# Kernel optimization log

Measured on AMD Instinct MI355X. Metric: run time of the kernel, lower is better.

Reference implementation:

```python
import jax, jax.numpy as jnp
import numpy as np

B, T, D = 2, 2048, 4096
H = 32            # query heads
HKV = 1           # kv heads (MQA; torch code requires HKV in {1, H})
HD = D // H       # head_dim = 128


def setup_inputs() -> dict:
    key = jax.random.key(0)
    ks = jax.random.split(key, 9)
    s = lambda fan_in: 1.0 / np.sqrt(fan_in)
    return {
        "x": jax.random.normal(ks[0], (B, T, D), dtype=jnp.float32),
        "wq_w": jax.random.normal(ks[1], (H * HD, D), dtype=jnp.float32) * s(D),
        "wq_b": jax.random.normal(ks[2], (H * HD,), dtype=jnp.float32) * 0.02,
        "wk_w": jax.random.normal(ks[3], (HKV * HD, D), dtype=jnp.float32) * s(D),
        "wk_b": jax.random.normal(ks[4], (HKV * HD,), dtype=jnp.float32) * 0.02,
        "wv_w": jax.random.normal(ks[5], (HKV * HD, D), dtype=jnp.float32) * s(D),
        "wv_b": jax.random.normal(ks[6], (HKV * HD,), dtype=jnp.float32) * 0.02,
        "wo_w": jax.random.normal(ks[7], (D, H * HD), dtype=jnp.float32) * s(H * HD),
        "wo_b": jax.random.normal(ks[8], (D,), dtype=jnp.float32) * 0.02,
    }


def reference(x, wq_w, wq_b, wk_w, wk_b, wv_w, wv_b, wo_w, wo_b):
    b, t, d = x.shape
    # projections (torch Linear: y = x @ W.T + b)
    q = (x @ wq_w.T + wq_b).reshape(b, t, H, HD)        # [B,T,H,hd]
    k = (x @ wk_w.T + wk_b).reshape(b, t, HKV, HD)      # [B,T,HKV,hd]
    v = (x @ wv_w.T + wv_b).reshape(b, t, HKV, HD)
    # MQA: squeeze the single kv head and broadcast across query heads
    k1 = k[:, :, 0, :]                                   # [B,T,hd]
    v1 = v[:, :, 0, :]
    scores = jnp.einsum("bqhd,bkd->bhqk", q, k1) / jnp.sqrt(jnp.float32(HD))
    causal = jnp.tril(jnp.ones((t, t), dtype=bool))      # keep lower triangle
    scores = jnp.where(causal, scores, -jnp.inf)
    weights = jax.nn.softmax(scores, axis=-1)            # [B,H,T,T]
    attn = jnp.einsum("bhqk,bkd->bqhd", weights, v1)     # [B,T,H,hd]
    attn = attn.reshape(b, t, H * HD)
    return attn @ wo_w.T + wo_b
```

## Files before the change

kernel.cpp:

```cpp
#include <hip/hip_runtime.h>

typedef unsigned short u16;
using bf16x8 = __attribute__((ext_vector_type(8))) __bf16;
using f32x4  = __attribute__((ext_vector_type(4))) float;


__device__ __forceinline__ u16 f2b(float f) {
    union { float f; unsigned int i; } x; x.f = f;
    unsigned int i = x.i + (((x.i >> 16) & 1u) + 0x7fffu);
    return (u16)(i >> 16);
}
__device__ __forceinline__ u16 f2b_ru(float f) {
    union { float f; unsigned int i; } x; x.f = f;
    return (u16)((x.i + 0x8000u) >> 16);
}
__device__ __forceinline__ void gload_lds16(const u16* g, u16* l) {
    __builtin_amdgcn_global_load_lds((const __attribute__((address_space(1))) void*)g,
                                     (__attribute__((address_space(3))) void*)l, 16, 0, 0);
}

__global__ __launch_bounds__(256) void cvt_f32_bf16(const float* __restrict__ in,
                                                    u16* __restrict__ out, int n) {
    int i = (blockIdx.x * 256 + threadIdx.x) * 8;
    if (i >= n) return;
    float4 a = *(const float4*)(in + i);
    float4 b = *(const float4*)(in + i + 4);
    union { u16 u[8]; uint4 v; } o;
    o.u[0] = f2b(a.x); o.u[1] = f2b(a.y); o.u[2] = f2b(a.z); o.u[3] = f2b(a.w);
    o.u[4] = f2b(b.x); o.u[5] = f2b(b.y); o.u[6] = f2b(b.z); o.u[7] = f2b(b.w);
    *(uint4*)(out + i) = o.v;
}


#define G_BAR()   __builtin_amdgcn_s_barrier()
#define G_LGKM0() asm volatile("s_waitcnt lgkmcnt(0)" ::: "memory")

struct GCtx {
    const u16* gA; const u16* gB;
    int fro;
    int dst;
    int wmi, wni;
    int rgA0, rgA1, rgB0, rgB1;
    int w;
};

__device__ __forceinline__ void stg2(const GCtx& c, const u16* gb, int rg, int kt, u16* sb) {
    const u16* src = gb + (size_t)rg * 65536 + (size_t)kt * 64;
    u16* d = sb + rg * 1024 + c.dst;
    gload_lds16(src,      d);
    gload_lds16(src + 32, d + 512);
}

template<int MODE>
__device__ __forceinline__ void tile_step(const GCtx& c, int u,
        u16* __restrict__ cA, u16* __restrict__ cB,
        u16* __restrict__ nA, u16* __restrict__ nB,
        f32x4 (&acc)[8][4]) {
    bf16x8 af[4][2], bf[2][2];
#pragma unroll
    for (int i = 0; i < 4; ++i) {
        const u16* p = cA + (((c.wmi * 8 + i) * 2) << 9) + c.fro;
        af[i][0] = *(const bf16x8*)(p);
        af[i][1] = *(const bf16x8*)(p + 512);
    }
#pragma unroll
    for (int n = 0; n < 2; ++n) {
        const u16* p = cB + (((c.wni * 4 + n) * 2) << 9) + c.fro;
        bf[n][0] = *(const bf16x8*)(p);
        bf[n][1] = *(const bf16x8*)(p + 512);
    }
    if (MODE < 2) stg2(c, c.gA, c.rgA1, u + 1, nA);
    G_BAR(); G_LGKM0();
    __builtin_amdgcn_s_setprio(1);
#pragma unroll
    for (int i = 0; i < 4; ++i)
#pragma unroll
        for (int n = 0; n < 2; ++n) {
            acc[i][n] = __builtin_amdgcn_mfma_f32_16x16x32_bf16(af[i][0], bf[n][0], acc[i][n], 0, 0, 0);
            acc[i][n] = __builtin_amdgcn_mfma_f32_16x16x32_bf16(af[i][1], bf[n][1], acc[i][n], 0, 0, 0);
        }
    __builtin_amdgcn_s_setprio(0);
    G_BAR();
#pragma unroll
    for (int n = 0; n < 2; ++n) {
        const u16* p = cB + (((c.wni * 4 + 2 + n) * 2) << 9) + c.fro;
        bf[n][0] = *(const bf16x8*)(p);
        bf[n][1] = *(const bf16x8*)(p + 512);
    }
    if (MODE < 2) stg2(c, c.gB, c.rgB0, u + 1, nB);
    G_BAR(); G_LGKM0();
    __builtin_amdgcn_s_setprio(1);
#pragma unroll
    for (int i = 0; i < 4; ++i)
#pragma unroll
        for (int n = 0; n < 2; ++n) {
            acc[i][2 + n] = __builtin_amdgcn_mfma_f32_16x16x32_bf16(af[i][0], bf[n][0], acc[i][2 + n], 0, 0, 0);
            acc[i][2 + n] = __builtin_amdgcn_mfma_f32_16x16x32_bf16(af[i][1], bf[n][1], acc[i][2 + n], 0, 0, 0);
        }
    __builtin_amdgcn_s_setprio(0);
    G_BAR();
#pragma unroll
    for (int i = 0; i < 4; ++i) {
        const u16* p = cA + (((c.wmi * 8 + 4 + i) * 2) << 9) + c.fro;
        af[i][0] = *(const bf16x8*)(p);
        af[i][1] = *(const bf16x8*)(p + 512);
    }
    if (MODE == 0) stg2(c, c.gA, c.rgA0, u + 2, cA);
    G_BAR(); G_LGKM0();
    __builtin_amdgcn_s_setprio(1);
#pragma unroll
    for (int i = 0; i < 4; ++i)
#pragma unroll
        for (int n = 0; n < 2; ++n) {
            acc[4 + i][2 + n] = __builtin_amdgcn_mfma_f32_16x16x32_bf16(af[i][0], bf[n][0], acc[4 + i][2 + n], 0, 0, 0);
            acc[4 + i][2 + n] = __builtin_amdgcn_mfma_f32_16x16x32_bf16(af[i][1], bf[n][1], acc[4 + i][2 + n], 0, 0, 0);
        }
    __builtin_amdgcn_s_setprio(0);
    G_BAR();
#pragma unroll
    for (int n = 0; n < 2; ++n) {
        const u16* p = cB + (((c.wni * 4 + n) * 2) << 9) + c.fro;
        bf[n][0] = *(const bf16x8*)(p);
        bf[n][1] = *(const bf16x8*)(p + 512);
    }
    if (MODE == 0) stg2(c, c.gB, c.rgB1, u + 2, cB);
    G_BAR(); G_LGKM0();
    __builtin_amdgcn_s_setprio(1);
#pragma unroll
    for (int i = 0; i < 4; ++i)
#pragma unroll
        for (int n = 0; n < 2; ++n) {
            acc[4 + i][n] = __builtin_amdgcn_mfma_f32_16x16x32_bf16(af[i][0], bf[n][0], acc[4 + i][n], 0, 0, 0);
            acc[4 + i][n] = __builtin_amdgcn_mfma_f32_16x16x32_bf16(af[i][1], bf[n][1], acc[4 + i][n], 0, 0, 0);
        }
    __builtin_amdgcn_s_setprio(0);
    if (MODE == 0) asm volatile("s_waitcnt vmcnt(4)" ::: "memory");
    if (MODE == 1) asm volatile("s_waitcnt vmcnt(0)" ::: "memory");
    G_BAR();
}

template<int NT>
__device__ __forceinline__ void gemm256(const u16* __restrict__ Ag,
                                        const u16* __restrict__ Bg,
                                        u16* __restrict__ lds,
                                        f32x4 (&acc)[8][4]) {
    const int t = threadIdx.x, l = t & 63, w = t >> 6;
    const int r = l & 15, qd = l >> 4, lr = l >> 2;
    const int co = ((l & 3) * 8) ^ (((l >> 5) & 1) << 4);
    GCtx c;
    c.w = w; c.wmi = w >> 2; c.wni = w & 3;
    c.gA = Ag + (size_t)lr * 4096 + co;
    c.gB = Bg + (size_t)lr * 4096 + co;
    c.fro = r * 32 + ((qd * 8) ^ (((r >> 3) & 1) << 4));
    c.dst = l * 8;
    c.rgA0 = (w & 3) | ((w & 4) << 1);
    c.rgA1 = c.rgA0 + 4;
    c.rgB0 = (w & 1) | ((w >> 1) << 2);
    c.rgB1 = c.rgB0 + 2;
    u16* sA0 = lds;          u16* sB0 = lds + 16384;
    u16* sA1 = lds + 32768;  u16* sB1 = lds + 49152;
#pragma unroll
    for (int i = 0; i < 8; ++i)
#pragma unroll
        for (int n = 0; n < 4; ++n) acc[i][n] = (f32x4){0.f, 0.f, 0.f, 0.f};
    stg2(c, c.gA, w, 0, sA0);     stg2(c, c.gA, w + 8, 0, sA0);
    stg2(c, c.gB, w, 0, sB0);     stg2(c, c.gB, w + 8, 0, sB0);
    stg2(c, c.gA, c.rgA0, 1, sA1);
    stg2(c, c.gB, c.rgB1, 1, sB1);
    asm volatile("s_waitcnt vmcnt(4)" ::: "memory");
    G_BAR();
#pragma unroll 1
    for (int u = 0; u + 2 < NT; u += 2) {
        tile_step<0>(c, u,     sA0, sB0, sA1, sB1, acc);
        tile_step<0>(c, u + 1, sA1, sB1, sA0, sB0, acc);
    }
    tile_step<1>(c, NT - 2, sA0, sB0, sA1, sB1, acc);
    tile_step<2>(c, NT - 1, sA1, sB1, sA0, sB0, acc);
}

__global__ __launch_bounds__(512, 2) void q_gemm(
    const u16* __restrict__ x, const u16* __restrict__ wq,
    const float* __restrict__ wqb, u16* __restrict__ Qb) {
    __shared__ __align__(16) u16 lds[65536];
    int bid = blockIdx.x;
    int wgid = (bid & 7) * 32 + (bid >> 3);
    int brow = wgid >> 4, bcol = wgid & 15;
    f32x4 acc[8][4];
    gemm256<64>(x + (size_t)brow * 256 * 4096, wq + (size_t)bcol * 256 * 4096, lds, acc);
    const int t = threadIdx.x, l = t & 63, w = t >> 6;
    const int wmi = w >> 2, wni = w & 3, r = l & 15, qd = l >> 4;
    const float QSCALE = 0.08838834764831845f * 1.4426950408889634f;
#pragma unroll
    for (int n = 0; n < 4; ++n) {
        int col = bcol * 256 + wni * 64 + n * 16 + r;
        float bv = wqb[col];
#pragma unroll
        for (int mt = 0; mt < 8; ++mt)
#pragma unroll
            for (int j = 0; j < 4; ++j) {
                int m = brow * 256 + wmi * 128 + mt * 16 + qd * 4 + j;
                Qb[(size_t)m * 4096 + col] = f2b((acc[mt][n][j] + bv) * QSCALE);
            }
    }
}

__global__ __launch_bounds__(512, 2) void kv_gemm(
    const u16* __restrict__ x, const u16* __restrict__ wkv,
    float* __restrict__ P) {
    __shared__ __align__(16) u16 lds[65536];
    int brow = blockIdx.x;
    int slice = blockIdx.y;
    f32x4 acc[8][4];
    gemm256<8>(x + (size_t)brow * 256 * 4096 + slice * 512,
               wkv + slice * 512, lds, acc);
    const int t = threadIdx.x, l = t & 63, w = t >> 6;
    const int wmi = w >> 2, wni = w & 3, r = l & 15, qd = l >> 4;
    float* Pb = P + (size_t)slice * 4096 * 256;
#pragma unroll
    for (int n = 0; n < 4; ++n) {
        int nl = wni * 64 + n * 16 + r;
#pragma unroll
        for (int mt = 0; mt < 8; ++mt)
#pragma unroll
            for (int j = 0; j < 4; ++j) {
                int m = brow * 256 + wmi * 128 + mt * 16 + qd * 4 + j;
                Pb[(size_t)m * 256 + nl] = acc[mt][n][j];
            }
    }
}

__global__ __launch_bounds__(256) void kv_reduce(const float* __restrict__ P,
        const float* __restrict__ wkb, const float* __restrict__ wvb,
        u16* __restrict__ Kb, u16* __restrict__ Vt) {
    int t = blockIdx.x * 256 + threadIdx.x;
    if (blockIdx.x < 2048) {
        int m = t >> 7, nl = t & 127;
        float s = 0.f;
#pragma unroll
        for (int sl = 0; sl < 8; ++sl) s += P[((size_t)sl * 4096 + m) * 256 + nl];
        Kb[(size_t)m * 128 + nl] = f2b(s + wkb[nl]);
    } else {
        int idx = t - 524288;
        int d = idx >> 12, m = idx & 4095;
        float s = 0.f;
#pragma unroll
        for (int sl = 0; sl < 8; ++sl) s += P[((size_t)sl * 4096 + m) * 256 + 128 + d];
        Vt[(size_t)d * 4096 + m] = f2b(s + wvb[d]);
    }
}

__global__ __launch_bounds__(512, 2) void out_gemm(
    const u16* __restrict__ A, const u16* __restrict__ W,
    const float* __restrict__ bias, float* __restrict__ C) {
    __shared__ __align__(16) u16 lds[65536];
    int bid = blockIdx.x;
    int wgid = (bid & 7) * 32 + (bid >> 3);
    int brow = wgid >> 4, bcol = wgid & 15;
    f32x4 acc[8][4];
    gemm256<64>(A + (size_t)brow * 256 * 4096, W + (size_t)bcol * 256 * 4096, lds, acc);
    const int t = threadIdx.x, l = t & 63, w = t >> 6;
    const int wmi = w >> 2, wni = w & 3, r = l & 15, qd = l >> 4;
#pragma unroll
    for (int n = 0; n < 4; ++n) {
        int col = bcol * 256 + wni * 64 + n * 16 + r;
        float bv = bias[col];
#pragma unroll
        for (int mt = 0; mt < 8; ++mt)
#pragma unroll
            for (int j = 0; j < 4; ++j) {
                int m = brow * 256 + wmi * 128 + mt * 16 + qd * 4 + j;
                C[(size_t)m * 4096 + col] = acc[mt][n][j] + bv;
            }
    }
}

__global__ __launch_bounds__(256, 2) void flash_mqa(
    const u16* __restrict__ Qb, const u16* __restrict__ Kb,
    const u16* __restrict__ Vt, u16* __restrict__ Ob) {
    __shared__ __align__(16) u16 sK[64 * 136];
    __shared__ __align__(16) u16 sV[128 * 72];
    __shared__ __align__(16) u16 sP[128 * 72];

    int t = threadIdx.x, lane = t & 63, w = t >> 6;
    int r = lane & 15, qd = lane >> 4;

    int fid = blockIdx.x + 16 * blockIdx.y + 512 * blockIdx.z;
    int qi  = 15 - (fid >> 6);
    int rem = fid & 63;
    int h   = rem & 31;
    size_t bt0 = (size_t)(rem >> 5) * 2048;
    int q0 = qi * 128;

    bf16x8 qf[2][4];
#pragma unroll
    for (int mt = 0; mt < 2; ++mt) {
        const u16* qp = Qb + (bt0 + q0 + w * 32 + mt * 16 + r) * 4096 + h * 128 + qd * 8;
#pragma unroll
        for (int kk = 0; kk < 4; ++kk) qf[mt][kk] = *(const bf16x8*)(qp + kk * 32);
    }

    f32x4 o[2][8], osum[2];
    float mrun[2][4];
#pragma unroll
    for (int mt = 0; mt < 2; ++mt) {
#pragma unroll
        for (int dn = 0; dn < 8; ++dn) o[mt][dn] = (f32x4){0.f, 0.f, 0.f, 0.f};
        osum[mt] = (f32x4){0.f, 0.f, 0.f, 0.f};
#pragma unroll
        for (int j = 0; j < 4; ++j) mrun[mt][j] = -1e30f;
    }

    union { uint4 v; bf16x8 b; } onesu;
    onesu.v = make_uint4(0x3F803F80u, 0x3F803F80u, 0x3F803F80u, 0x3F803F80u);
    const bf16x8 ones = onesu.b;

    int e = t * 8;
    int krr = e >> 7, kcc = e & 127;
    int vdd = e >> 6, vkv = e & 63;
    int ktiles = 2 * qi + 2;

    for (int kt = 0; kt < ktiles; ++kt) {
        int kb = kt * 64;
        const u16* kg = Kb + (bt0 + kb + krr) * 128 + kcc;
        u16* kl = sK + krr * 136 + kcc;
#pragma unroll
        for (int c = 0; c < 4; ++c)
            *(uint4*)(kl + c * 16 * 136) = *(const uint4*)(kg + (size_t)c * 16 * 128);
        const u16* vg = Vt + (size_t)vdd * 4096 + bt0 + kb + vkv;
        u16* vl = sV + vdd * 72 + vkv;
#pragma unroll
        for (int c = 0; c < 4; ++c)
            *(uint4*)(vl + c * 32 * 72) = *(const uint4*)(vg + (size_t)c * 32 * 4096);
        __syncthreads();

        f32x4 s[2][4];
#pragma unroll
        for (int mt = 0; mt < 2; ++mt)
#pragma unroll
            for (int nt = 0; nt < 4; ++nt) s[mt][nt] = (f32x4){0.f, 0.f, 0.f, 0.f};
#pragma unroll
        for (int kk = 0; kk < 4; ++kk) {
            bf16x8 kf[4];
#pragma unroll
            for (int nt = 0; nt < 4; ++nt)
                kf[nt] = *(const bf16x8*)(sK + (nt * 16 + r) * 136 + kk * 32 + qd * 8);
#pragma unroll
            for (int mt = 0; mt < 2; ++mt)
#pragma unroll
                for (int nt = 0; nt < 4; ++nt)
                    s[mt][nt] = __builtin_amdgcn_mfma_f32_16x16x32_bf16(qf[mt][kk], kf[nt], s[mt][nt], 0, 0, 0);
        }

#pragma unroll
        for (int mt = 0; mt < 2; ++mt) {
            int qrow0 = q0 + w * 32 + mt * 16 + qd * 4;
#pragma unroll
            for (int nt = 0; nt < 4; ++nt) {
                int kcol = kb + nt * 16 + r;
#pragma unroll
                for (int j = 0; j < 4; ++j)
                    s[mt][nt][j] = (kcol <= qrow0 + j) ? s[mt][nt][j] : -1e30f;
            }
#pragma unroll
            for (int j = 0; j < 4; ++j) {
                float mx = fmaxf(fmaxf(s[mt][0][j], s[mt][1][j]), fmaxf(s[mt][2][j], s[mt][3][j]));
                mx = fmaxf(mx, __shfl_xor(mx, 1));
                mx = fmaxf(mx, __shfl_xor(mx, 2));
                mx = fmaxf(mx, __shfl_xor(mx, 4));
                mx = fmaxf(mx, __shfl_xor(mx, 8));
                float mnew = fmaxf(mrun[mt][j], mx);
                float alpha = exp2f(mrun[mt][j] - mnew);
                mrun[mt][j] = mnew;
                u16* pp = sP + (size_t)(w * 32 + mt * 16 + qd * 4 + j) * 72;
#pragma unroll
                for (int nt = 0; nt < 4; ++nt)
                    pp[nt * 16 + r] = f2b_ru(exp2f(s[mt][nt][j] - mnew));
#pragma unroll
                for (int dn = 0; dn < 8; ++dn) o[mt][dn][j] *= alpha;
                osum[mt][j] *= alpha;
            }
        }

        __syncthreads();

#pragma unroll
        for (int kk = 0; kk < 2; ++kk) {
            bf16x8 pf[2];
#pragma unroll
            for (int mt = 0; mt < 2; ++mt) {
                pf[mt] = *(const bf16x8*)(sP + (w * 32 + mt * 16 + r) * 72 + kk * 32 + qd * 8);
                osum[mt] = __builtin_amdgcn_mfma_f32_16x16x32_bf16(pf[mt], ones, osum[mt], 0, 0, 0);
            }
#pragma unroll
            for (int dn = 0; dn < 8; ++dn) {
                bf16x8 vf = *(const bf16x8*)(sV + (dn * 16 + r) * 72 + kk * 32 + qd * 8);
#pragma unroll
                for (int mt = 0; mt < 2; ++mt)
                    o[mt][dn] = __builtin_amdgcn_mfma_f32_16x16x32_bf16(pf[mt], vf, o[mt][dn], 0, 0, 0);
            }
        }
        __syncthreads();
    }

#pragma unroll
    for (int mt = 0; mt < 2; ++mt)
#pragma unroll
        for (int j = 0; j < 4; ++j) {
            float inv = 1.0f / osum[mt][j];
            u16* op = Ob + (bt0 + q0 + w * 32 + mt * 16 + qd * 4 + j) * 4096 + h * 128;
#pragma unroll
            for (int dn = 0; dn < 8; ++dn) op[dn * 16 + r] = f2b(o[mt][dn][j] * inv);
        }
}

extern "C" void kernel_launch(void* const* d_in, const int* in_sizes, int n_in,
                              void* d_out, int out_size, void* d_ws, size_t ws_size,
                              hipStream_t stream) {
    const float* x   = (const float*)d_in[0];
    const float* wq  = (const float*)d_in[1];
    const float* wqb = (const float*)d_in[2];
    const float* wk  = (const float*)d_in[3];
    const float* wkb = (const float*)d_in[4];
    const float* wv  = (const float*)d_in[5];
    const float* wvb = (const float*)d_in[6];
    const float* wo  = (const float*)d_in[7];
    const float* wob = (const float*)d_in[8];

    const int NX = 4096 * 4096;
    const int NK = 128 * 4096;

    u16* xb   = (u16*)d_ws;
    u16* wq16 = xb   + (size_t)NX;
    u16* wk16 = wq16 + (size_t)NX;
    u16* wv16 = wk16 + (size_t)NK;
    u16* Qb   = wv16 + (size_t)NK;
    u16* Kb   = Qb   + (size_t)NX;
    u16* Vt   = Kb   + (size_t)NK;
    u16* Ob   = xb;
    u16* wo16 = wq16;
    float* Pf = (float*)Qb;
    float* out = (float*)d_out;

    cvt_f32_bf16<<<NX / 2048, 256, 0, stream>>>(x,  xb,   NX);
    cvt_f32_bf16<<<NX / 2048, 256, 0, stream>>>(wq, wq16, NX);
    cvt_f32_bf16<<<NK / 2048, 256, 0, stream>>>(wk, wk16, NK);
    cvt_f32_bf16<<<NK / 2048, 256, 0, stream>>>(wv, wv16, NK);

    kv_gemm<<<dim3(16, 8), 512, 0, stream>>>(xb, wk16, Pf);
    kv_reduce<<<4096, 256, 0, stream>>>(Pf, wkb, wvb, Kb, Vt);
    q_gemm<<<256, 512, 0, stream>>>(xb, wq16, wqb, Qb);

    cvt_f32_bf16<<<NX / 2048, 256, 0, stream>>>(wo, wo16, NX);

    flash_mqa<<<dim3(16, 32, 2), 256, 0, stream>>>(Qb, Kb, Vt, Ob);
    out_gemm<<<256, 512, 0, stream>>>(Ob, wo16, wob, out);
}
```

Before: 629.0 us.

## Transpose QK^T MFMA, add lazy rescale threshold, drop mid-tile barrier

Swaps the MFMA operand order so each lane holds one query row's scores, which cuts the row max to two cross-lane shuffles. Output rescaling is skipped unless some row's max grows past the running max by a threshold, so the per-tile alpha multiplies usually go away. P is written with packed 8-byte stores. The block-wide barrier before the PV phase is replaced by an lgkmcnt wait, which is valid only because each wave reads back just its own P rows. Adds s_setprio around the MFMA sections, and the lazy rescale can let exp values exceed 1 in bf16.

```diff
diff --git a/kernel.cpp b/kernel.cpp
--- a/kernel.cpp
+++ b/kernel.cpp
@@ -9,10 +9,6 @@
     union { float f; unsigned int i; } x; x.f = f;
     unsigned int i = x.i + (((x.i >> 16) & 1u) + 0x7fffu);
     return (u16)(i >> 16);
-}
-__device__ __forceinline__ u16 f2b_ru(float f) {
-    union { float f; unsigned int i; } x; x.f = f;
-    return (u16)((x.i + 0x8000u) >> 16);
 }
 __device__ __forceinline__ void gload_lds16(const u16* g, u16* l) {
     __builtin_amdgcn_global_load_lds((const __attribute__((address_space(1))) void*)g,
@@ -300,14 +296,13 @@
     }
 
     f32x4 o[2][8], osum[2];
-    float mrun[2][4];
+    float mrun[2];
 #pragma unroll
     for (int mt = 0; mt < 2; ++mt) {
 #pragma unroll
         for (int dn = 0; dn < 8; ++dn) o[mt][dn] = (f32x4){0.f, 0.f, 0.f, 0.f};
         osum[mt] = (f32x4){0.f, 0.f, 0.f, 0.f};
-#pragma unroll
-        for (int j = 0; j < 4; ++j) mrun[mt][j] = -1e30f;
+        mrun[mt] = -1e30f;
     }
 
     union { uint4 v; bf16x8 b; } onesu;
@@ -318,6 +313,7 @@
     int krr = e >> 7, kcc = e & 127;
     int vdd = e >> 6, vkv = e & 63;
     int ktiles = 2 * qi + 2;
+    const float THR = 8.0f;
 
     for (int kt = 0; kt < ktiles; ++kt) {
         int kb = kt * 64;
@@ -333,11 +329,12 @@
             *(uint4*)(vl + c * 32 * 72) = *(const uint4*)(vg + (size_t)c * 32 * 4096);
         __syncthreads();
 
-        f32x4 s[2][4];
+        f32x4 s2[2][4];
 #pragma unroll
         for (int mt = 0; mt < 2; ++mt)
 #pragma unroll
-            for (int nt = 0; nt < 4; ++nt) s[mt][nt] = (f32x4){0.f, 0.f, 0.f, 0.f};
+            for (int nt = 0; nt < 4; ++nt) s2[mt][nt] = (f32x4){0.f, 0.f, 0.f, 0.f};
+        __builtin_amdgcn_s_setprio(1);
 #pragma unroll
         for (int kk = 0; kk < 4; ++kk) {
             bf16x8 kf[4];
@@ -348,41 +345,65 @@
             for (int mt = 0; mt < 2; ++mt)
 #pragma unroll
                 for (int nt = 0; nt < 4; ++nt)
-                    s[mt][nt] = __builtin_amdgcn_mfma_f32_16x16x32_bf16(qf[mt][kk], kf[nt], s[mt][nt], 0, 0, 0);
-        }
-
+                    s2[mt][nt] = __builtin_amdgcn_mfma_f32_16x16x32_bf16(kf[nt], qf[mt][kk], s2[mt][nt], 0, 0, 0);
+        }
+        __builtin_amdgcn_s_setprio(0);
+
+        float mx[2];
+        bool need = false;
 #pragma unroll
         for (int mt = 0; mt < 2; ++mt) {
-            int qrow0 = q0 + w * 32 + mt * 16 + qd * 4;
+            int qg = q0 + w * 32 + mt * 16 + r;
+            int kvb = kb + qd * 4;
+#pragma unroll
+            for (int nt = 0; nt < 4; ++nt)
+#pragma unroll
+                for (int j = 0; j < 4; ++j)
+                    s2[mt][nt][j] = (kvb + nt * 16 + j <= qg) ? s2[mt][nt][j] : -1e30f;
+            f32x4 vm;
+#pragma unroll
+            for (int j = 0; j < 4; ++j)
+                vm[j] = fmaxf(fmaxf(s2[mt][0][j], s2[mt][1][j]), fmaxf(s2[mt][2][j], s2[mt][3][j]));
+            float m0 = fmaxf(fmaxf(vm[0], vm[1]), fmaxf(vm[2], vm[3]));
+            m0 = fmaxf(m0, __shfl_xor(m0, 16));
+            m0 = fmaxf(m0, __shfl_xor(m0, 32));
+            mx[mt] = m0;
+            need = need || (m0 > mrun[mt] + THR);
+        }
+
+        if (__any(need)) {
+#pragma unroll
+            for (int mt = 0; mt < 2; ++mt) {
+                float mnew = fmaxf(mrun[mt], mx[mt]);
+                float al = exp2f(mrun[mt] - mnew);
+                mrun[mt] = mnew;
+#pragma unroll
+                for (int j = 0; j < 4; ++j) {
+                    float aj = __shfl(al, ((lane >> 4) << 2) + j);
+#pragma unroll
+                    for (int dn = 0; dn < 8; ++dn) o[mt][dn][j] *= aj;
+                    osum[mt][j] *= aj;
+                }
+            }
+        }
+
+#pragma unroll
+        for (int mt = 0; mt < 2; ++mt) {
+            u16* pp = sP + (size_t)(w * 32 + mt * 16 + r) * 72 + qd * 4;
 #pragma unroll
             for (int nt = 0; nt < 4; ++nt) {
-                int kcol = kb + nt * 16 + r;
+                union { __bf16 b[4]; uint2 u; } pk;
 #pragma unroll
                 for (int j = 0; j < 4; ++j)
-                    s[mt][nt][j] = (kcol <= qrow0 + j) ? s[mt][nt][j] : -1e30f;
-            }
-#pragma unroll
-            for (int j = 0; j < 4; ++j) {
-                float mx = fmaxf(fmaxf(s[mt][0][j], s[mt][1][j]), fmaxf(s[mt][2][j], s[mt][3][j]));
-                mx = fmaxf(mx, __shfl_xor(mx, 1));
-                mx = fmaxf(mx, __shfl_xor(mx, 2));
-                mx = fmaxf(mx, __shfl_xor(mx, 4));
-                mx = fmaxf(mx, __shfl_xor(mx, 8));
-                float mnew = fmaxf(mrun[mt][j], mx);
-                float alpha = exp2f(mrun[mt][j] - mnew);
-                mrun[mt][j] = mnew;
-                u16* pp = sP + (size_t)(w * 32 + mt * 16 + qd * 4 + j) * 72;
-#pragma unroll
-                for (int nt = 0; nt < 4; ++nt)
-                    pp[nt * 16 + r] = f2b_ru(exp2f(s[mt][nt][j] - mnew));
-#pragma unroll
-                for (int dn = 0; dn < 8; ++dn) o[mt][dn][j] *= alpha;
-                osum[mt][j] *= alpha;
-            }
-        }
-
-        __syncthreads();
-
+                    pk.b[j] = (__bf16)exp2f(s2[mt][nt][j] - mrun[mt]);
+                *(uint2*)(pp + nt * 16) = pk.u;
+            }
+        }
+
+        asm volatile("s_waitcnt lgkmcnt(0)" ::: "memory");
+        __builtin_amdgcn_sched_barrier(0);
+
+        __builtin_amdgcn_s_setprio(1);
 #pragma unroll
         for (int kk = 0; kk < 2; ++kk) {
             bf16x8 pf[2];
@@ -399,6 +420,7 @@
                     o[mt][dn] = __builtin_amdgcn_mfma_f32_16x16x32_bf16(pf[mt], vf, o[mt][dn], 0, 0, 0);
             }
         }
+        __builtin_amdgcn_s_setprio(0);
         __syncthreads();
     }
 
```

Result: faster. 591.6 us (-5.9%).
